# Performance work log

Hardware: AMD Instinct MI355X
Metric: run time of the kernel (lower is better)

## Reference

```python
import jax, jax.numpy as jnp
import numpy as np

SMOOTHING = 0.1
IGNORE_INDEX = 0


def setup_inputs() -> dict:
    key = jax.random.key(0)
    k1, k2 = jax.random.split(key)
    B, L, V = 4, 2048, 32000
    # probabilities (module takes probs and applies torch.log itself);
    # normalize uniform draws over vocab so rows are valid prob distributions
    p = jax.random.uniform(k1, (B, L, V), dtype=jnp.float32, minval=1e-3, maxval=1.0)
    p = p / p.sum(axis=-1, keepdims=True)
    targets = jax.random.randint(k2, (B, L), 0, V, dtype=jnp.int64 if jax.config.jax_enable_x64 else jnp.int32)
    return {"inputs": p, "targets": targets, "norm": B * L}


def reference(inputs, targets, norm):
    # KLDiv(log p, q) with q = onehot*(1-s) + s/V, summed over vocab,
    # masked where targets == ignore_index, summed and divided by norm.
    # sum_v q_v*(log q_v - log p_v) computed without materializing the one-hot:
    V = inputs.shape[-1]
    s = SMOOTHING
    a = s / V                 # off-target prob
    b = 1.0 - s + a           # on-target prob
    logp = jnp.log(inputs)                                   # [B,L,V]
    logp_t = jnp.take_along_axis(logp, targets[..., None], axis=-1)[..., 0]  # [B,L]
    sum_logp = logp.sum(axis=-1)                             # [B,L]
    const = a * np.log(a) * (V - 1) + b * np.log(b)          # entropy-like constant
    loss = const - a * (sum_logp - logp_t) - b * logp_t      # [B,L]
    loss = jnp.where(targets == IGNORE_INDEX, 0.0, loss)
    return loss.sum() / norm
```

## Files before the change

### kernel.cpp

```cpp
#include <hip/hip_runtime.h>
#include <cmath>


#define LS_LN2 0.6931471805599453094172321214581766

template<int N4C, int STRIDE_C>
__global__ __launch_bounds__(256) void ls_flat_log2sum(
    const float* __restrict__ p,
    float*       __restrict__ partA,
    int n4_rt)
{
    const int n4     = (N4C      > 0) ? N4C      : n4_rt;
    const int stride = (STRIDE_C > 0) ? STRIDE_C : (int)(gridDim.x * blockDim.x);
    const float4* __restrict__ p4 = (const float4*)p;

    float s0 = 0.f, s1 = 0.f, s2 = 0.f, s3 = 0.f;
    #pragma unroll 5
    for (int i = blockIdx.x * 256 + threadIdx.x; i < n4; i += stride) {
        float4 v = p4[i];
        s0 += __log2f(v.x);
        s1 += __log2f(v.y);
        s2 += __log2f(v.z);
        s3 += __log2f(v.w);
    }
    float s = (s0 + s1) + (s2 + s3);

    #pragma unroll
    for (int off = 32; off > 0; off >>= 1)
        s += __shfl_down(s, off, 64);

    __shared__ float wsum[4];
    const int wid  = threadIdx.x >> 6;
    const int lane = threadIdx.x & 63;
    if (lane == 0) wsum[wid] = s;
    __syncthreads();
    if (threadIdx.x == 0)
        partA[blockIdx.x] = (wsum[0] + wsum[1]) + (wsum[2] + wsum[3]);
}

__global__ __launch_bounds__(256) void ls_row_terms(
    const float* __restrict__ p,
    const int*   __restrict__ tgt,
    float*       __restrict__ partB,
    float cterm, float bma, float a_ln2,
    int BL, int V)
{
    __shared__ int   masked[256];
    __shared__ int   nmaskS;
    __shared__ float wsum[4];
    if (threadIdx.x == 0) nmaskS = 0;
    __syncthreads();

    const int r = blockIdx.x * 256 + threadIdx.x;
    float my = 0.f;
    if (r < BL) {
        const int t = tgt[r];
        if (t != 0) {
            my = cterm - bma * __logf(p[(size_t)r * V + t]);
        } else {
            masked[atomicAdd(&nmaskS, 1)] = r;
        }
    }
    __syncthreads();

    const int nm = nmaskS;
    for (int m = 0; m < nm; ++m) {
        const int row = masked[m];
        const float4* p4 = (const float4*)(p + (size_t)row * V);
        float s = 0.f;
        for (int i = threadIdx.x; i < (V >> 2); i += 256) {
            float4 v = p4[i];
            s += __log2f(v.x) + __log2f(v.y) + __log2f(v.z) + __log2f(v.w);
        }
        my += a_ln2 * s;
    }

    #pragma unroll
    for (int off = 32; off > 0; off >>= 1)
        my += __shfl_down(my, off, 64);
    const int wid  = threadIdx.x >> 6;
    const int lane = threadIdx.x & 63;
    if (lane == 0) wsum[wid] = my;
    __syncthreads();
    if (threadIdx.x == 0)
        partB[blockIdx.x] = (wsum[0] + wsum[1]) + (wsum[2] + wsum[3]);
}

__global__ __launch_bounds__(256) void ls_reduce_finalize(
    const float* __restrict__ partA, int nA, float neg_a_ln2,
    const float* __restrict__ partB, int nB,
    const int*   __restrict__ normp,
    float*       __restrict__ out)
{
    double s = 0.0;
    for (int i = threadIdx.x; i < nA; i += 256)
        s += (double)neg_a_ln2 * (double)partA[i];
    for (int i = threadIdx.x; i < nB; i += 256)
        s += (double)partB[i];

    #pragma unroll
    for (int off = 32; off > 0; off >>= 1)
        s += __shfl_down(s, off, 64);

    __shared__ double wsum[4];
    const int wid  = threadIdx.x >> 6;
    const int lane = threadIdx.x & 63;
    if (lane == 0) wsum[wid] = s;
    __syncthreads();
    if (threadIdx.x == 0) {
        double tot = ((wsum[0] + wsum[1]) + (wsum[2] + wsum[3]));
        const int   ni = normp[0];
        const float nf = (ni > 0 && ni < (1 << 30)) ? (float)ni : __int_as_float(ni);
        out[0] = (float)(tot / (double)nf);
    }
}

template<int NV4>
__global__ __launch_bounds__(256) void ls_row_kernel(
    const float* __restrict__ p,
    const int*   __restrict__ tgt,
    const int*   __restrict__ normp,
    float*       __restrict__ out,
    float cterm, int V, int nv4_rt)
{
    const int row = blockIdx.x;
    const int tid = threadIdx.x;
    const int t   = tgt[row];
    if (t == 0) return;

    const float*  prow = p + (size_t)row * (size_t)V;
    const float4* p4   = (const float4*)prow;
    const int     nv4  = (NV4 > 0) ? NV4 : nv4_rt;

    float s0 = 0.f, s1 = 0.f, s2 = 0.f, s3 = 0.f;
    #pragma unroll 4
    for (int i = tid; i < nv4; i += 256) {
        float4 v = p4[i];
        s0 += __logf(v.x);
        s1 += __logf(v.y);
        s2 += __logf(v.z);
        s3 += __logf(v.w);
    }
    float s = (s0 + s1) + (s2 + s3);
    #pragma unroll
    for (int off = 32; off > 0; off >>= 1)
        s += __shfl_down(s, off, 64);

    __shared__ float wsum[4];
    const int wid  = tid >> 6;
    const int lane = tid & 63;
    if (lane == 0) wsum[wid] = s;
    __syncthreads();

    if (tid == 0) {
        float tot = (wsum[0] + wsum[1]) + (wsum[2] + wsum[3]);
        float lt  = __logf(prow[t]);
        const float a = 0.1f / (float)V;
        const float b = 1.0f - 0.1f + a;
        float loss = cterm - a * (tot - lt) - b * lt;
        int   ni = normp[0];
        float nf = (ni > 0 && ni < (1 << 30)) ? (float)ni : __int_as_float(ni);
        atomicAdd(out, loss / nf);
    }
}

extern "C" void kernel_launch(void* const* d_in, const int* in_sizes, int n_in,
                              void* d_out, int out_size, void* d_ws, size_t ws_size,
                              hipStream_t stream) {
    const float* p     = (const float*)d_in[0];
    const int*   tgt   = (const int*)d_in[1];
    const int*   normp = (const int*)d_in[2];
    float*       out   = (float*)d_out;

    const int BL = in_sizes[1];
    const int V  = in_sizes[0] / in_sizes[1];

    const double a = 0.1 / (double)V;
    const double b = 1.0 - 0.1 + a;
    const float  cterm     = (float)(a * log(a) * (double)(V - 1) + b * log(b));
    const float  bma       = (float)(b - a);
    const float  a_ln2     = (float)(a * LS_LN2);
    const float  neg_a_ln2 = -a_ln2;

    const int       NA   = 2048;
    const int       NB   = (BL + 255) / 256;
    const long long n4ll = (long long)BL * (long long)(V >> 2);
    const size_t    need = (size_t)(NA + NB) * sizeof(float);

    if ((V & 3) == 0 && ws_size >= need && n4ll < (1LL << 31)) {
        float* partA = (float*)d_ws;
        float* partB = partA + NA;

        if (V == 32000 && BL == 8192) {
            ls_flat_log2sum<65536000, 2048 * 256>
                <<<NA, 256, 0, stream>>>(p, partA, 0);
        } else {
            ls_flat_log2sum<0, 0>
                <<<NA, 256, 0, stream>>>(p, partA, (int)n4ll);
        }
        ls_row_terms<<<NB, 256, 0, stream>>>(
            p, tgt, partB, cterm, bma, a_ln2, BL, V);
        ls_reduce_finalize<<<1, 256, 0, stream>>>(
            partA, NA, neg_a_ln2, partB, NB, normp, out);
    } else {
        hipMemsetAsync(d_out, 0, sizeof(float), stream);
        ls_row_kernel<0><<<BL, 256, 0, stream>>>(p, tgt, normp, out, cterm, V, V >> 2);
    }
}
```

Baseline: 1.297 ms.

## Replace per-element log2 with exponent sum plus log2 of mantissa products

Splits each float into its exponent and mantissa, sums the exponents as integers and multiplies mantissas in groups of 20 (fast path) or 4 (fallback), so only one log2 runs per group instead of one per element. The fast path is rewritten around a fixed 25-iteration unrolled body with five strided loads issued together, aiming to turn the compute-bound log loop into a memory-bound one. The masked-row path now uses the same trick. The fallback path is rewired to reuse the three-kernel scheme with a single-block sum and an empty if-block, which looks sloppy. Precision may drop slightly from the mantissa product, and denormals or zero inputs are handled differently.

```diff
diff --git a/kernel.cpp b/kernel.cpp
--- a/kernel.cpp
+++ b/kernel.cpp
@@ -4,26 +4,76 @@
 
 #define LS_LN2 0.6931471805599453094172321214581766
 
-template<int N4C, int STRIDE_C>
-__global__ __launch_bounds__(256) void ls_flat_log2sum(
+__device__ __forceinline__ float ls_mant(unsigned u) {
+    return __uint_as_float((u & 0x7FFFFFu) | 0x3F800000u);
+}
+
+template<int BODIES, int STRIDE>
+__global__ __launch_bounds__(256) void ls_flat_prodlog(
+    const uint4* __restrict__ p4,
+    float*       __restrict__ partA)
+{
+    int   i    = blockIdx.x * 256 + threadIdx.x;
+    float slog = 0.f;
+    int   ecnt = 0;
+
+    #pragma unroll 2
+    for (int b = 0; b < BODIES; ++b) {
+        const uint4 a0 = p4[i];
+        const uint4 a1 = p4[i +     STRIDE];
+        const uint4 a2 = p4[i + 2 * STRIDE];
+        const uint4 a3 = p4[i + 3 * STRIDE];
+        const uint4 a4 = p4[i + 4 * STRIDE];
+        i += 5 * STRIDE;
+
+        ecnt += (int)((a0.x >> 23) + (a0.y >> 23) + (a0.z >> 23) + (a0.w >> 23)
+                    + (a1.x >> 23) + (a1.y >> 23) + (a1.z >> 23) + (a1.w >> 23)
+                    + (a2.x >> 23) + (a2.y >> 23) + (a2.z >> 23) + (a2.w >> 23)
+                    + (a3.x >> 23) + (a3.y >> 23) + (a3.z >> 23) + (a3.w >> 23)
+                    + (a4.x >> 23) + (a4.y >> 23) + (a4.z >> 23) + (a4.w >> 23));
+
+        const float p0 = (ls_mant(a0.x) * ls_mant(a0.y)) * (ls_mant(a0.z) * ls_mant(a0.w));
+        const float p1 = (ls_mant(a1.x) * ls_mant(a1.y)) * (ls_mant(a1.z) * ls_mant(a1.w));
+        const float p2 = (ls_mant(a2.x) * ls_mant(a2.y)) * (ls_mant(a2.z) * ls_mant(a2.w));
+        const float p3 = (ls_mant(a3.x) * ls_mant(a3.y)) * (ls_mant(a3.z) * ls_mant(a3.w));
+        const float p4v= (ls_mant(a4.x) * ls_mant(a4.y)) * (ls_mant(a4.z) * ls_mant(a4.w));
+        const float P  = ((p0 * p1) * (p2 * p3)) * p4v;
+
+        slog += __log2f(P);
+    }
+
+    float s = slog + (float)(ecnt - BODIES * 20 * 127);
+
+    #pragma unroll
+    for (int off = 32; off > 0; off >>= 1)
+        s += __shfl_down(s, off, 64);
+
+    __shared__ float wsum[4];
+    const int wid  = threadIdx.x >> 6;
+    const int lane = threadIdx.x & 63;
+    if (lane == 0) wsum[wid] = s;
+    __syncthreads();
+    if (threadIdx.x == 0)
+        partA[blockIdx.x] = (wsum[0] + wsum[1]) + (wsum[2] + wsum[3]);
+}
+
+__global__ __launch_bounds__(256) void ls_flat_log2sum_rt(
     const float* __restrict__ p,
     float*       __restrict__ partA,
-    int n4_rt)
-{
-    const int n4     = (N4C      > 0) ? N4C      : n4_rt;
-    const int stride = (STRIDE_C > 0) ? STRIDE_C : (int)(gridDim.x * blockDim.x);
-    const float4* __restrict__ p4 = (const float4*)p;
-
-    float s0 = 0.f, s1 = 0.f, s2 = 0.f, s3 = 0.f;
-    #pragma unroll 5
+    int n4)
+{
+    const int stride = (int)(gridDim.x * blockDim.x);
+    const uint4* __restrict__ p4 = (const uint4*)p;
+
+    float slog = 0.f;
+    int   ecnt = 0;
     for (int i = blockIdx.x * 256 + threadIdx.x; i < n4; i += stride) {
-        float4 v = p4[i];
-        s0 += __log2f(v.x);
-        s1 += __log2f(v.y);
-        s2 += __log2f(v.z);
-        s3 += __log2f(v.w);
-    }
-    float s = (s0 + s1) + (s2 + s3);
+        uint4 a = p4[i];
+        ecnt += (int)((a.x >> 23) + (a.y >> 23) + (a.z >> 23) + (a.w >> 23)) - 508;
+        float P = (ls_mant(a.x) * ls_mant(a.y)) * (ls_mant(a.z) * ls_mant(a.w));
+        slog += __log2f(P);
+    }
+    float s = slog + (float)ecnt;
 
     #pragma unroll
     for (int off = 32; off > 0; off >>= 1)
@@ -66,13 +116,16 @@
     const int nm = nmaskS;
     for (int m = 0; m < nm; ++m) {
         const int row = masked[m];
-        const float4* p4 = (const float4*)(p + (size_t)row * V);
+        const uint4* p4 = (const uint4*)(p + (size_t)row * V);
         float s = 0.f;
+        int   e = 0;
         for (int i = threadIdx.x; i < (V >> 2); i += 256) {
-            float4 v = p4[i];
-            s += __log2f(v.x) + __log2f(v.y) + __log2f(v.z) + __log2f(v.w);
-        }
-        my += a_ln2 * s;
+            uint4 a = p4[i];
+            e += (int)((a.x >> 23) + (a.y >> 23) + (a.z >> 23) + (a.w >> 23)) - 508;
+            float P = (ls_mant(a.x) * ls_mant(a.y)) * (ls_mant(a.z) * ls_mant(a.w));
+            s += __log2f(P);
+        }
+        my += a_ln2 * (s + (float)e);
     }
 
     #pragma unroll
@@ -112,55 +165,6 @@
         const int   ni = normp[0];
         const float nf = (ni > 0 && ni < (1 << 30)) ? (float)ni : __int_as_float(ni);
         out[0] = (float)(tot / (double)nf);
-    }
-}
-
-template<int NV4>
-__global__ __launch_bounds__(256) void ls_row_kernel(
-    const float* __restrict__ p,
-    const int*   __restrict__ tgt,
-    const int*   __restrict__ normp,
-    float*       __restrict__ out,
-    float cterm, int V, int nv4_rt)
-{
-    const int row = blockIdx.x;
-    const int tid = threadIdx.x;
-    const int t   = tgt[row];
-    if (t == 0) return;
-
-    const float*  prow = p + (size_t)row * (size_t)V;
-    const float4* p4   = (const float4*)prow;
-    const int     nv4  = (NV4 > 0) ? NV4 : nv4_rt;
-
-    float s0 = 0.f, s1 = 0.f, s2 = 0.f, s3 = 0.f;
-    #pragma unroll 4
-    for (int i = tid; i < nv4; i += 256) {
-        float4 v = p4[i];
-        s0 += __logf(v.x);
-        s1 += __logf(v.y);
-        s2 += __logf(v.z);
-        s3 += __logf(v.w);
-    }
-    float s = (s0 + s1) + (s2 + s3);
-    #pragma unroll
-    for (int off = 32; off > 0; off >>= 1)
-        s += __shfl_down(s, off, 64);
-
-    __shared__ float wsum[4];
-    const int wid  = tid >> 6;
-    const int lane = tid & 63;
-    if (lane == 0) wsum[wid] = s;
-    __syncthreads();
-
-    if (tid == 0) {
-        float tot = (wsum[0] + wsum[1]) + (wsum[2] + wsum[3]);
-        float lt  = __logf(prow[t]);
-        const float a = 0.1f / (float)V;
-        const float b = 1.0f - 0.1f + a;
-        float loss = cterm - a * (tot - lt) - b * lt;
-        int   ni = normp[0];
-        float nf = (ni > 0 && ni < (1 << 30)) ? (float)ni : __int_as_float(ni);
-        atomicAdd(out, loss / nf);
     }
 }
 
@@ -192,11 +196,10 @@
         float* partB = partA + NA;
 
         if (V == 32000 && BL == 8192) {
-            ls_flat_log2sum<65536000, 2048 * 256>
-                <<<NA, 256, 0, stream>>>(p, partA, 0);
+            ls_flat_prodlog<25, 2048 * 256>
+                <<<NA, 256, 0, stream>>>((const uint4*)p, partA);
         } else {
-            ls_flat_log2sum<0, 0>
-                <<<NA, 256, 0, stream>>>(p, partA, (int)n4ll);
+            ls_flat_log2sum_rt<<<NA, 256, 0, stream>>>(p, partA, (int)n4ll);
         }
         ls_row_terms<<<NB, 256, 0, stream>>>(
             p, tgt, partB, cterm, bma, a_ln2, BL, V);
@@ -204,6 +207,11 @@
             partA, NA, neg_a_ln2, partB, NB, normp, out);
     } else {
         hipMemsetAsync(d_out, 0, sizeof(float), stream);
-        ls_row_kernel<0><<<BL, 256, 0, stream>>>(p, tgt, normp, out, cterm, V, V >> 2);
-    }
-}
+        if ((V & 3) == 0 && ws_size >= need && n4ll < (1LL << 31)) {
+        }
+        ls_flat_log2sum_rt<<<1, 256, 0, stream>>>(p, (float*)d_ws, (int)n4ll);
+        ls_row_terms<<<NB, 256, 0, stream>>>(p, tgt, (float*)d_ws + 1, cterm, bma, a_ln2, BL, V);
+        ls_reduce_finalize<<<1, 256, 0, stream>>>((float*)d_ws, 1, neg_a_ln2,
+                                                  (float*)d_ws + 1, NB, normp, out);
+    }
+}
```

Result: no change. 1.304 ms (+0.5%).
